# Kernel tuning notes

Measured on AMD Instinct MI355X. Metric: run time of the kernel, lower is better.

## Reference

```python
import jax, jax.numpy as jnp
import numpy as np

E = 8       # num_experts
C = 1024    # output_dim (== input_dim, so no input_proj)


def setup_inputs() -> dict:
    key = jax.random.key(0)
    ks = jax.random.split(key, 8)
    B, N = 4, 2048
    s = 0.02
    return {
        "x":    jax.random.normal(ks[0], (B, N, C), jnp.float32),
        "x_ir": jax.random.normal(ks[1], (B, N, C), jnp.float32),
        # expert Linear weights, torch layout (out, in) per expert -> (E, C, C)
        "We": jax.random.normal(ks[2], (E, C, C), jnp.float32) * s,
        "be": jax.random.normal(ks[3], (E, C), jnp.float32) * s,
        # gate: Linear(C, C//2) -> ReLU -> Linear(C//2, E)
        "gw1": jax.random.normal(ks[4], (C // 2, C), jnp.float32) * s,
        "gb1": jax.random.normal(ks[5], (C // 2,), jnp.float32) * s,
        "gw2": jax.random.normal(ks[6], (E, C // 2), jnp.float32) * s,
        "gb2": jax.random.normal(ks[7], (E,), jnp.float32) * s,
    }


def _gates(x, gw1, gb1, gw2, gb2):
    gx = x.mean(axis=1)                                   # [B, C]
    h = jax.nn.relu(gx @ gw1.T + gb1)                     # [B, C//2]
    return jax.nn.softmax(h @ gw2.T + gb2, axis=-1)       # [B, E]


def _moe(x, We, be, g):
    # Equivalent to sum_e g[b,e] * (x @ We[e].T + be[e]); since experts are
    # linear, fold gates into a per-batch weight matrix (compute-efficient).
    Wb = jnp.einsum("be,eoc->boc", g, We)                 # [B, O, C]
    bb = g @ be                                           # [B, O]
    return jnp.einsum("bnc,boc->bno", x, Wb) + bb[:, None, :]


def reference(x, x_ir, We, be, gw1, gb1, gw2, gb2):
    g = _gates(x, gw1, gb1, gw2, gb2)                     # gates computed from x only
    moe_x = _moe(x, We, be, g)
    moe_x_ir = _moe(x_ir, We, be, g)
    return (moe_x, moe_x_ir)
```

## Files before the change

kernel.cpp:

```cpp
#include <hip/hip_runtime.h>
#include <hip/hip_bf16.h>
#include <stdint.h>

#define B_  4
#define N_  2048
#define C_  1024
#define E_  8
#define H_  512

typedef __bf16 bf16x8 __attribute__((ext_vector_type(8)));
typedef __bf16 bf16x4 __attribute__((ext_vector_type(4)));
typedef float  f32x4  __attribute__((ext_vector_type(4)));

#define WB_OFF   0ull
#define XB_OFF   (8ull*1024*1024)
#define GX_OFF   (XB_OFF + 32ull*1024*1024)
#define G_OFF    (GX_OFF + 4096ull*4)
#define BB_OFF   (G_OFF + 128ull)
#define H_OFF    (BB_OFF + 4096ull*4)

__device__ __forceinline__ void gload16(const void* g, void* l) {
  __builtin_amdgcn_global_load_lds((const __attribute__((address_space(1))) void*)g,
                                   (__attribute__((address_space(3))) void*)l, 16, 0, 0);
}

__global__ void cast2_kernel(const float* __restrict__ x, const float* __restrict__ x_ir,
                             __bf16* __restrict__ dst) {
  size_t i = (size_t)blockIdx.x * 256 + threadIdx.x;
  const size_t half = (size_t)B_ * N_ * C_ / 8;
  const float* src = (i < half) ? x : x_ir;
  size_t li = (i < half) ? i : i - half;
  const float4* s = (const float4*)src + li * 2;
  float4 a = s[0], b = s[1];
  bf16x8 o;
  o[0] = (__bf16)a.x; o[1] = (__bf16)a.y; o[2] = (__bf16)a.z; o[3] = (__bf16)a.w;
  o[4] = (__bf16)b.x; o[5] = (__bf16)b.y; o[6] = (__bf16)b.z; o[7] = (__bf16)b.w;
  *(bf16x8*)(dst + i * 8) = o;
}

__global__ void mean_kernel(const float* __restrict__ x, float* __restrict__ gx) {
  int b = blockIdx.z, cs = blockIdx.y, ns = blockIdx.x;
  int c = cs * 256 + threadIdx.x;
  const float* p = x + ((size_t)b * N_ + (size_t)ns * 64) * C_ + c;
  float s = 0.f;
  #pragma unroll 8
  for (int n = 0; n < 64; ++n) s += p[(size_t)n * C_];
  atomicAdd(&gx[b * C_ + c], s * (1.0f / N_));
}

__global__ void h_kernel(const float* __restrict__ gx, const float* __restrict__ gw1,
                         const float* __restrict__ gb1, float* __restrict__ h) {
  __shared__ float sgx[B_][C_];
  int t = threadIdx.x;
  for (int i = t; i < B_ * C_; i += 256) sgx[i >> 10][i & 1023] = gx[i];
  __syncthreads();
  int j = blockIdx.x * 64 + (t >> 2);
  int b = t & 3;
  const float4* row = (const float4*)(gw1 + (size_t)j * C_);
  float acc = 0.f;
  #pragma unroll 4
  for (int c4 = 0; c4 < C_ / 4; ++c4) {
    float4 w = row[c4];
    acc += w.x * sgx[b][c4*4+0] + w.y * sgx[b][c4*4+1]
         + w.z * sgx[b][c4*4+2] + w.w * sgx[b][c4*4+3];
  }
  h[b * H_ + j] = fmaxf(acc + gb1[j], 0.f);
}

__global__ __launch_bounds__(512) void gate2_kernel(const float* __restrict__ h,
    const float* __restrict__ gw2, const float* __restrict__ gb2,
    const float* __restrict__ be, float* __restrict__ g, float* __restrict__ bbp) {
  __shared__ float slog[B_ * E_];
  __shared__ float sg[B_ * E_];
  int t = threadIdx.x, wv = t >> 6, lane = t & 63;
  for (int q = 0; q < 4; ++q) {
    int pi = wv * 4 + q;
    int b = pi >> 3, e = pi & 7;
    float s = 0.f;
    for (int k = lane; k < H_; k += 64) s += h[b * H_ + k] * gw2[e * H_ + k];
    for (int off = 32; off; off >>= 1) s += __shfl_down(s, off);
    if (lane == 0) slog[pi] = s + gb2[e];
  }
  __syncthreads();
  if (t < B_) {
    float m = -1e30f;
    for (int e = 0; e < E_; ++e) m = fmaxf(m, slog[t * E_ + e]);
    float p[E_], sum = 0.f;
    for (int e = 0; e < E_; ++e) { p[e] = __expf(slog[t * E_ + e] - m); sum += p[e]; }
    float inv = 1.f / sum;
    for (int e = 0; e < E_; ++e) { sg[t * E_ + e] = p[e] * inv; g[t * E_ + e] = p[e] * inv; }
  }
  __syncthreads();
  #pragma unroll
  for (int q = 0; q < 8; ++q) {
    int i = q * 512 + t;
    int b = i >> 10, o = i & 1023;
    float s = 0.f;
    #pragma unroll
    for (int e = 0; e < E_; ++e) s += sg[b * E_ + e] * be[e * C_ + o];
    bbp[i] = s;
  }
}

__global__ void wb_kernel(const float* __restrict__ g, const float* __restrict__ We,
                          __bf16* __restrict__ Wb) {
  size_t i = (size_t)blockIdx.x * 256 + threadIdx.x;
  int b = (int)(i >> 18);
  size_t oc4 = i & ((1u << 18) - 1);
  float gl[E_];
  #pragma unroll
  for (int e = 0; e < E_; ++e) gl[e] = g[b * E_ + e];
  const float4* src = (const float4*)We + oc4;
  float4 acc = make_float4(0.f, 0.f, 0.f, 0.f);
  #pragma unroll
  for (int e = 0; e < E_; ++e) {
    float4 w = src[(size_t)e * (C_ * C_ / 4)];
    acc.x += gl[e] * w.x; acc.y += gl[e] * w.y;
    acc.z += gl[e] * w.z; acc.w += gl[e] * w.w;
  }
  bf16x4 o;
  o[0] = (__bf16)acc.x; o[1] = (__bf16)acc.y; o[2] = (__bf16)acc.z; o[3] = (__bf16)acc.w;
  *(bf16x4*)(Wb + i * 4) = o;
}

#define NT 16

__global__ __launch_bounds__(512, 2) void moe_gemm(const __bf16* __restrict__ Xb,
    const __bf16* __restrict__ Wb, const float* __restrict__ bb, float* __restrict__ out) {
  __shared__ __attribute__((aligned(128))) char smem[2][65536];

  const int t = threadIdx.x;
  const int wid = t >> 6, lane = t & 63;
  const int wm = wid >> 2, wn = wid & 3;

  int f = blockIdx.x;
  int swz = (f & 7) * 32 + (f >> 3);
  int xb_ = swz & 3, yb_ = (swz >> 2) & 7, z = swz >> 5;
  int b = z & 3;
  const size_t mat = (size_t)N_ * C_;
  const __bf16* A  = Xb + (size_t)z * mat;
  const __bf16* Bm = Wb + (size_t)b * C_ * C_;
  float* O = out + (size_t)z * mat;
  const int row0 = yb_ * 256, col0 = xb_ * 256;

  const int lrow8 = lane >> 3;
  const int kblk  = ((lane & 7) ^ lrow8) << 3;

  const int lr = lane & 15;
  const int swzk0 = (((lane >> 4) + 0) ^ (lane & 7)) << 4;
  const int swzk1 = (((lane >> 4) + 4) ^ (lane & 7)) << 4;

  auto stage = [&](int sid, int k0, char* buf) {
    #pragma unroll
    for (int j = 0; j < 2; ++j) {
      int u = wid * 2 + j;
      int rl0 = u * 8;
      if (sid == 0 || sid == 3) {
        int hh = (sid == 3) ? 1 : 0;
        int row_u = rl0 + (rl0 & 64) + hh * 64;
        const __bf16* src = A + (size_t)(row0 + row_u + lrow8) * C_ + k0 + kblk;
        gload16(src, buf + row_u * 128);
      } else {
        int hh = (sid == 2) ? 1 : 0;
        int col_u = (rl0 & 31) + (rl0 >> 5) * 64 + hh * 32;
        const __bf16* src = Bm + (size_t)(col0 + col_u + lrow8) * C_ + k0 + kblk;
        gload16(src, buf + 32768 + col_u * 128);
      }
    }
  };

  f32x4 acc[8][4] = {};
  bf16x8 av[4][2];
  bf16x8 bv[2][2][2];

  #pragma unroll
  for (int sid = 0; sid < 4; ++sid) stage(sid, 0, smem[0]);
  asm volatile("s_waitcnt vmcnt(4)" ::: "memory");
  __builtin_amdgcn_s_barrier();

  for (int kt = 0; kt < NT; ++kt) {
    char* rb = smem[kt & 1];
    char* wbuf = smem[(kt + 1) & 1];
    const char* rbA = rb;
    const char* rbB = rb + 32768;
    const bool more = (kt + 1 < NT);
    const int knext = (kt + 1) * 64;

    #pragma unroll
    for (int p = 0; p < 4; ++p) {
      const int Aq = p >> 1, Bq = p & 1;
      if (p == 0 || p == 2) {
        #pragma unroll
        for (int mq = 0; mq < 4; ++mq) {
          int rby = (wm * 128 + Aq * 64 + mq * 16 + lr) * 128;
          av[mq][0] = *(const bf16x8*)(rbA + rby + swzk0);
          av[mq][1] = *(const bf16x8*)(rbA + rby + swzk1);
        }
      }
      if (p == 0 || p == 1) {
        #pragma unroll
        for (int nq = 0; nq < 2; ++nq) {
          int cby = (wn * 64 + Bq * 32 + nq * 16 + lr) * 128;
          bv[Bq][nq][0] = *(const bf16x8*)(rbB + cby + swzk0);
          bv[Bq][nq][1] = *(const bf16x8*)(rbB + cby + swzk1);
        }
      }
      if (more) stage(p, knext, wbuf);
      if (p < 3) {
        asm volatile("s_waitcnt lgkmcnt(0)" ::: "memory");
        __builtin_amdgcn_sched_barrier(0);
      }
      __builtin_amdgcn_s_setprio(1);
      #pragma unroll
      for (int mq = 0; mq < 4; ++mq)
        #pragma unroll
        for (int nq = 0; nq < 2; ++nq) {
          acc[Aq*4+mq][Bq*2+nq] = __builtin_amdgcn_mfma_f32_16x16x32_bf16(
              av[mq][0], bv[Bq][nq][0], acc[Aq*4+mq][Bq*2+nq], 0, 0, 0);
          acc[Aq*4+mq][Bq*2+nq] = __builtin_amdgcn_mfma_f32_16x16x32_bf16(
              av[mq][1], bv[Bq][nq][1], acc[Aq*4+mq][Bq*2+nq], 0, 0, 0);
        }
      __builtin_amdgcn_s_setprio(0);
      if (more) {
        if (p == 2) asm volatile("s_waitcnt vmcnt(6)" ::: "memory");
        else        asm volatile("s_waitcnt vmcnt(4)" ::: "memory");
      } else {
        if (p == 0)      asm volatile("s_waitcnt vmcnt(2)" ::: "memory");
        else if (p == 1) asm volatile("s_waitcnt vmcnt(0)" ::: "memory");
      }
      __builtin_amdgcn_s_barrier();
    }
  }

  float* eb = (float*)(smem[0]) + wid * (16 * 68);
  const int er = lane >> 4;
  const f32x4 bias4 = *(const f32x4*)(bb + b * C_ + col0 + wn * 64 + lr * 4);

  #pragma unroll
  for (int m = 0; m < 8; ++m) {
    #pragma unroll
    for (int n = 0; n < 4; ++n) {
      f32x4 v = acc[m][n];
      #pragma unroll
      for (int r = 0; r < 4; ++r)
        eb[(er * 4 + r) * 68 + n * 16 + lr] = v[r];
    }
    asm volatile("s_waitcnt lgkmcnt(0)" ::: "memory");
    __builtin_amdgcn_sched_barrier(0);
    #pragma unroll
    for (int j = 0; j < 4; ++j) {
      int row = j * 4 + er;
      f32x4 v = *(const f32x4*)(eb + row * 68 + lr * 4);
      v[0] += bias4[0]; v[1] += bias4[1]; v[2] += bias4[2]; v[3] += bias4[3];
      int grow = row0 + wm * 128 + m * 16 + row;
      int gcol = col0 + wn * 64 + lr * 4;
      *(f32x4*)(O + (size_t)grow * C_ + gcol) = v;
    }
  }
}

extern "C" void kernel_launch(void* const* d_in, const int* in_sizes, int n_in,
                              void* d_out, int out_size, void* d_ws, size_t ws_size,
                              hipStream_t stream) {
  const float* x    = (const float*)d_in[0];
  const float* x_ir = (const float*)d_in[1];
  const float* We   = (const float*)d_in[2];
  const float* be   = (const float*)d_in[3];
  const float* gw1  = (const float*)d_in[4];
  const float* gb1  = (const float*)d_in[5];
  const float* gw2  = (const float*)d_in[6];
  const float* gb2  = (const float*)d_in[7];
  float* out = (float*)d_out;

  char* ws = (char*)d_ws;
  __bf16* Wb  = (__bf16*)(ws + WB_OFF);
  __bf16* Xb  = (__bf16*)(ws + XB_OFF);
  float*  gx  = (float*)(ws + GX_OFF);
  float*  g   = (float*)(ws + G_OFF);
  float*  bbp = (float*)(ws + BB_OFF);
  float*  h   = (float*)(ws + H_OFF);

  hipMemsetAsync(gx, 0, B_ * C_ * sizeof(float), stream);

  cast2_kernel<<<8192, 256, 0, stream>>>(x, x_ir, Xb);
  mean_kernel<<<dim3(32, 4, 4), 256, 0, stream>>>(x, gx);
  h_kernel<<<8, 256, 0, stream>>>(gx, gw1, gb1, h);
  gate2_kernel<<<1, 512, 0, stream>>>(h, gw2, gb2, be, g, bbp);
  wb_kernel<<<4096, 256, 0, stream>>>(g, We, Wb);

  moe_gemm<<<256, 512, 0, stream>>>(Xb, Wb, bbp, out);
}
```

Baseline: 111.8 us.

## Fuse cast with mean reduction and rework GEMM k-loop into three-phase pipeline

Merges the bf16 cast of x/x_ir and the per-batch mean of x into one kernel, so x is read from HBM once instead of twice and a launch is removed. The MoE GEMM main loop is rescheduled from four uniform sub-steps into three phases. A operands are double-buffered in registers and LDS reads are interleaved with MFMAs, with fewer barriers and waitcnts per k-tile. This adds register pressure from the doubled A fragments, and the hand-placed vmcnt counts must match the stage issue order.

```diff
diff --git a/kernel.cpp b/kernel.cpp
--- a/kernel.cpp
+++ b/kernel.cpp
@@ -24,28 +24,42 @@
                                    (__attribute__((address_space(3))) void*)l, 16, 0, 0);
 }
 
-__global__ void cast2_kernel(const float* __restrict__ x, const float* __restrict__ x_ir,
-                             __bf16* __restrict__ dst) {
-  size_t i = (size_t)blockIdx.x * 256 + threadIdx.x;
-  const size_t half = (size_t)B_ * N_ * C_ / 8;
-  const float* src = (i < half) ? x : x_ir;
-  size_t li = (i < half) ? i : i - half;
-  const float4* s = (const float4*)src + li * 2;
-  float4 a = s[0], b = s[1];
-  bf16x8 o;
-  o[0] = (__bf16)a.x; o[1] = (__bf16)a.y; o[2] = (__bf16)a.z; o[3] = (__bf16)a.w;
-  o[4] = (__bf16)b.x; o[5] = (__bf16)b.y; o[6] = (__bf16)b.z; o[7] = (__bf16)b.w;
-  *(bf16x8*)(dst + i * 8) = o;
-}
-
-__global__ void mean_kernel(const float* __restrict__ x, float* __restrict__ gx) {
-  int b = blockIdx.z, cs = blockIdx.y, ns = blockIdx.x;
-  int c = cs * 256 + threadIdx.x;
-  const float* p = x + ((size_t)b * N_ + (size_t)ns * 64) * C_ + c;
-  float s = 0.f;
-  #pragma unroll 8
-  for (int n = 0; n < 64; ++n) s += p[(size_t)n * C_];
-  atomicAdd(&gx[b * C_ + c], s * (1.0f / N_));
+#define CFENCE() asm volatile("" ::: "memory")
+
+__global__ __launch_bounds__(256) void castmean_kernel(const float* __restrict__ x,
+    const float* __restrict__ x_ir, __bf16* __restrict__ dst, float* __restrict__ gx) {
+  __shared__ float red[256][8];
+  int bi = blockIdx.x;
+  int half = bi >> 8, rblk = bi & 255;
+  const float* src = half ? x_ir : x;
+  int t = threadIdx.x;
+  int cg = t & 127, rg = t >> 7;
+  int r0 = rblk * 32 + rg * 16;
+  const float4* sp = (const float4*)(src + (size_t)r0 * C_) + cg * 2;
+  __bf16* dp = dst + (size_t)half * ((size_t)B_ * N_ * C_) + (size_t)r0 * C_ + cg * 8;
+  float s[8] = {};
+  #pragma unroll 4
+  for (int rr = 0; rr < 16; ++rr) {
+    float4 a = sp[0], b4 = sp[1];
+    bf16x8 o;
+    o[0] = (__bf16)a.x; o[1] = (__bf16)a.y; o[2] = (__bf16)a.z; o[3] = (__bf16)a.w;
+    o[4] = (__bf16)b4.x; o[5] = (__bf16)b4.y; o[6] = (__bf16)b4.z; o[7] = (__bf16)b4.w;
+    *(bf16x8*)dp = o;
+    s[0] += a.x; s[1] += a.y; s[2] += a.z; s[3] += a.w;
+    s[4] += b4.x; s[5] += b4.y; s[6] += b4.z; s[7] += b4.w;
+    sp += C_ / 4; dp += C_;
+  }
+  if (half == 0) {
+    #pragma unroll
+    for (int j = 0; j < 8; ++j) red[t][j] = s[j];
+    __syncthreads();
+    if (t < 128) {
+      int b = (rblk * 32) >> 11;
+      #pragma unroll
+      for (int j = 0; j < 8; ++j)
+        atomicAdd(&gx[b * C_ + cg * 8 + j], (red[t][j] + red[t + 128][j]) * (1.0f / N_));
+    }
+  }
 }
 
 __global__ void h_kernel(const float* __restrict__ gx, const float* __restrict__ gw1,
@@ -170,66 +184,71 @@
   };
 
   f32x4 acc[8][4] = {};
-  bf16x8 av[4][2];
+  bf16x8 av[2][4][2];
   bf16x8 bv[2][2][2];
 
+  #define RD_A(buf_, Aq_, mq_) { \
+    int rby = (wm * 128 + (Aq_) * 64 + (mq_) * 16 + lr) * 128; \
+    av[buf_][mq_][0] = *(const bf16x8*)(rbA + rby + swzk0); \
+    av[buf_][mq_][1] = *(const bf16x8*)(rbA + rby + swzk1); }
+  #define RD_B(Bq_, nq_) { \
+    int cby = (wn * 64 + (Bq_) * 32 + (nq_) * 16 + lr) * 128; \
+    bv[Bq_][nq_][0] = *(const bf16x8*)(rbB + cby + swzk0); \
+    bv[Bq_][nq_][1] = *(const bf16x8*)(rbB + cby + swzk1); }
+  #define MFMA1(ab_, mq_, Bq_, nq_) { \
+    acc[(ab_)*4+(mq_)][(Bq_)*2+(nq_)] = __builtin_amdgcn_mfma_f32_16x16x32_bf16( \
+        av[ab_][mq_][0], bv[Bq_][nq_][0], acc[(ab_)*4+(mq_)][(Bq_)*2+(nq_)], 0, 0, 0); \
+    acc[(ab_)*4+(mq_)][(Bq_)*2+(nq_)] = __builtin_amdgcn_mfma_f32_16x16x32_bf16( \
+        av[ab_][mq_][1], bv[Bq_][nq_][1], acc[(ab_)*4+(mq_)][(Bq_)*2+(nq_)], 0, 0, 0); }
+
   #pragma unroll
   for (int sid = 0; sid < 4; ++sid) stage(sid, 0, smem[0]);
-  asm volatile("s_waitcnt vmcnt(4)" ::: "memory");
+  asm volatile("s_waitcnt vmcnt(2)" ::: "memory");
   __builtin_amdgcn_s_barrier();
+  CFENCE();
 
   for (int kt = 0; kt < NT; ++kt) {
-    char* rb = smem[kt & 1];
+    const char* rbA = smem[kt & 1];
+    const char* rbB = rbA + 32768;
     char* wbuf = smem[(kt + 1) & 1];
-    const char* rbA = rb;
-    const char* rbB = rb + 32768;
     const bool more = (kt + 1 < NT);
     const int knext = (kt + 1) * 64;
 
-    #pragma unroll
-    for (int p = 0; p < 4; ++p) {
-      const int Aq = p >> 1, Bq = p & 1;
-      if (p == 0 || p == 2) {
-        #pragma unroll
-        for (int mq = 0; mq < 4; ++mq) {
-          int rby = (wm * 128 + Aq * 64 + mq * 16 + lr) * 128;
-          av[mq][0] = *(const bf16x8*)(rbA + rby + swzk0);
-          av[mq][1] = *(const bf16x8*)(rbA + rby + swzk1);
-        }
-      }
-      if (p == 0 || p == 1) {
-        #pragma unroll
-        for (int nq = 0; nq < 2; ++nq) {
-          int cby = (wn * 64 + Bq * 32 + nq * 16 + lr) * 128;
-          bv[Bq][nq][0] = *(const bf16x8*)(rbB + cby + swzk0);
-          bv[Bq][nq][1] = *(const bf16x8*)(rbB + cby + swzk1);
-        }
-      }
-      if (more) stage(p, knext, wbuf);
-      if (p < 3) {
-        asm volatile("s_waitcnt lgkmcnt(0)" ::: "memory");
-        __builtin_amdgcn_sched_barrier(0);
-      }
-      __builtin_amdgcn_s_setprio(1);
-      #pragma unroll
-      for (int mq = 0; mq < 4; ++mq)
-        #pragma unroll
-        for (int nq = 0; nq < 2; ++nq) {
-          acc[Aq*4+mq][Bq*2+nq] = __builtin_amdgcn_mfma_f32_16x16x32_bf16(
-              av[mq][0], bv[Bq][nq][0], acc[Aq*4+mq][Bq*2+nq], 0, 0, 0);
-          acc[Aq*4+mq][Bq*2+nq] = __builtin_amdgcn_mfma_f32_16x16x32_bf16(
-              av[mq][1], bv[Bq][nq][1], acc[Aq*4+mq][Bq*2+nq], 0, 0, 0);
-        }
-      __builtin_amdgcn_s_setprio(0);
-      if (more) {
-        if (p == 2) asm volatile("s_waitcnt vmcnt(6)" ::: "memory");
-        else        asm volatile("s_waitcnt vmcnt(4)" ::: "memory");
-      } else {
-        if (p == 0)      asm volatile("s_waitcnt vmcnt(2)" ::: "memory");
-        else if (p == 1) asm volatile("s_waitcnt vmcnt(0)" ::: "memory");
-      }
-      __builtin_amdgcn_s_barrier();
-    }
+    if (more) { stage(0, knext, wbuf); stage(1, knext, wbuf); }
+    RD_A(0, 0, 0) RD_B(0, 0) RD_A(0, 0, 1) RD_B(0, 1) RD_A(0, 0, 2) RD_A(0, 0, 3)
+    __builtin_amdgcn_s_setprio(1);
+    MFMA1(0, 0, 0, 0) MFMA1(0, 0, 0, 1)
+    RD_B(1, 0) RD_B(1, 1)
+    MFMA1(0, 1, 0, 0) MFMA1(0, 1, 0, 1)
+    MFMA1(0, 2, 0, 0) MFMA1(0, 2, 0, 1)
+    MFMA1(0, 3, 0, 0) MFMA1(0, 3, 0, 1)
+    __builtin_amdgcn_s_setprio(0);
+    if (more) asm volatile("s_waitcnt vmcnt(4)" ::: "memory");
+    else      asm volatile("s_waitcnt vmcnt(0)" ::: "memory");
+    __builtin_amdgcn_s_barrier();
+    CFENCE();
+
+    if (more) { stage(2, knext, wbuf); stage(3, knext, wbuf); }
+    __builtin_amdgcn_s_setprio(1);
+    MFMA1(0, 0, 1, 0) MFMA1(0, 0, 1, 1)
+    RD_A(1, 1, 0) RD_A(1, 1, 1)
+    MFMA1(0, 1, 1, 0) MFMA1(0, 1, 1, 1)
+    RD_A(1, 1, 2) RD_A(1, 1, 3)
+    MFMA1(0, 2, 1, 0) MFMA1(0, 2, 1, 1)
+    MFMA1(0, 3, 1, 0) MFMA1(0, 3, 1, 1)
+    __builtin_amdgcn_s_setprio(0);
+    __builtin_amdgcn_s_barrier();
+    CFENCE();
+
+    __builtin_amdgcn_s_setprio(1);
+    MFMA1(1, 0, 0, 0) MFMA1(1, 0, 0, 1) MFMA1(1, 1, 0, 0) MFMA1(1, 1, 0, 1)
+    MFMA1(1, 2, 0, 0) MFMA1(1, 2, 0, 1) MFMA1(1, 3, 0, 0) MFMA1(1, 3, 0, 1)
+    MFMA1(1, 0, 1, 0) MFMA1(1, 0, 1, 1) MFMA1(1, 1, 1, 0) MFMA1(1, 1, 1, 1)
+    MFMA1(1, 2, 1, 0) MFMA1(1, 2, 1, 1) MFMA1(1, 3, 1, 0) MFMA1(1, 3, 1, 1)
+    __builtin_amdgcn_s_setprio(0);
+    if (more) asm volatile("s_waitcnt vmcnt(2)" ::: "memory");
+    __builtin_amdgcn_s_barrier();
+    CFENCE();
   }
 
   float* eb = (float*)(smem[0]) + wid * (16 * 68);
@@ -282,8 +301,7 @@
 
   hipMemsetAsync(gx, 0, B_ * C_ * sizeof(float), stream);
 
-  cast2_kernel<<<8192, 256, 0, stream>>>(x, x_ir, Xb);
-  mean_kernel<<<dim3(32, 4, 4), 256, 0, stream>>>(x, gx);
+  castmean_kernel<<<512, 256, 0, stream>>>(x, x_ir, Xb, gx);
   h_kernel<<<8, 256, 0, stream>>>(gx, gw1, gb1, h);
   gate2_kernel<<<1, 512, 0, stream>>>(h, gw2, gb2, be, g, bbp);
   wb_kernel<<<4096, 256, 0, stream>>>(g, We, Wb);
```

Result: slower. 115.4 us (+3.2%).
